# Kernel tuning notes

Measured on AMD Instinct MI355X. Metric: run time of the kernel, lower is better.

The kernel has to match this reference:

```python
import jax, jax.numpy as jnp
import numpy as np
import math

B, H, S, D = 2, 16, 2048, 128

def setup_inputs() -> dict:
    key = jax.random.key(0)
    kq, kk, kv, km = jax.random.split(key, 4)
    q = jax.random.normal(kq, (B, H, S, D), dtype=jnp.float32)
    k = jax.random.normal(kk, (B, H, S, D), dtype=jnp.float32)
    v = jax.random.normal(kv, (B, H, S, D), dtype=jnp.float32)
    mask = jax.random.randint(km, (1, 1, S, S), 0, 2, dtype=jnp.int32)
    return {"q": q, "k": k, "v": v, "mask": mask}

def reference(q, k, v, mask):
    head_dim = q.shape[-1]
    # scores: [B,H,Sq,Sk]
    scores = jnp.einsum('bhqd,bhkd->bhqk', q, k) / math.sqrt(head_dim)
    scores = jnp.where(mask == 0, jnp.float32(-1e10), scores)
    attn = jax.nn.softmax(scores, axis=-1)
    out = jnp.einsum('bhqk,bhkd->bhqd', attn, v)
    return out, attn
```

## Files before the change

kernel.cpp:

```cpp
#include <hip/hip_runtime.h>
#include <hip/hip_bf16.h>
#include <stdint.h>

#define SDIM 2048
#define DDIM 128
#define NKT  64

typedef __bf16 bf16x8 __attribute__((ext_vector_type(8)));
typedef float  f32x16 __attribute__((ext_vector_type(16)));

__global__ void build_bits_kernel(const int* __restrict__ mask, uint32_t* __restrict__ bitsT) {
  const int id   = blockIdx.x * 4 + (threadIdx.x >> 6);
  const int lane = threadIdx.x & 63;
  const int row  = id >> 5;
  const int kc   = id & 31;
  const int m = mask[(size_t)row * SDIM + kc * 64 + lane];
  const unsigned long long b = __ballot(m != 0);
  if (lane == 0)  bitsT[(size_t)(kc * 2    ) * SDIM + row] = (uint32_t)(b & 0xffffffffull);
  if (lane == 32) bitsT[(size_t)(kc * 2 + 1) * SDIM + row] = (uint32_t)(b >> 32);
}

__launch_bounds__(256, 2)
__global__ void attn_kernel(const float* __restrict__ qg, const float* __restrict__ kg,
                            const float* __restrict__ vg, const uint32_t* __restrict__ bitsT,
                            float* __restrict__ outg, float* __restrict__ attng) {
  __shared__ __align__(16) __bf16 KR[32 * 128];
  __shared__ __align__(16) __bf16 VTR[128 * 32];
  __shared__ __align__(16) __bf16 PR[4][32 * 32];
  __shared__ uint32_t MW[128];

  const int bid  = blockIdx.x;
  const int swzb = (bid & 7) * 64 + (bid >> 3);
  const int head = swzb >> 4;
  const int qb   = swzb & 15;
  const int tid  = threadIdx.x;
  const int wv   = tid >> 6;
  const int lane = tid & 63;
  const int col  = lane & 31;
  const int hi   = lane >> 5;

  const float* qh = qg + (size_t)head * SDIM * DDIM;
  const float* kh = kg + (size_t)head * SDIM * DDIM;
  const float* vh = vg + (size_t)head * SDIM * DDIM;
  float* outh  = outg  + (size_t)head * SDIM * DDIM;
  float* attnh = attng + (size_t)head * SDIM * SDIM;

  const int qrow0 = qb * 128 + wv * 32;
  const float cscale = 1.4426950408889634f * 0.08838834764831845f;
  const uint32_t lanebit = 1u << col;

  const int str = tid & 31;
  const int sdb = (tid >> 5) * 16;

  int rowl[16];
#pragma unroll
  for (int r = 0; r < 16; ++r) rowl[r] = wv * 32 + (r & 3) + 8 * (r >> 2) + 4 * hi;

  auto stage_k = [&](int kt) {
    const float* src = kh + (size_t)(kt * 32 + str) * DDIM + sdb;
    float4 a0 = *(const float4*)(src + 0);
    float4 a1 = *(const float4*)(src + 4);
    float4 a2 = *(const float4*)(src + 8);
    float4 a3 = *(const float4*)(src + 12);
    bf16x8 w0, w1;
    w0[0]=(__bf16)a0.x; w0[1]=(__bf16)a0.y; w0[2]=(__bf16)a0.z; w0[3]=(__bf16)a0.w;
    w0[4]=(__bf16)a1.x; w0[5]=(__bf16)a1.y; w0[6]=(__bf16)a1.z; w0[7]=(__bf16)a1.w;
    w1[0]=(__bf16)a2.x; w1[1]=(__bf16)a2.y; w1[2]=(__bf16)a2.z; w1[3]=(__bf16)a2.w;
    w1[4]=(__bf16)a3.x; w1[5]=(__bf16)a3.y; w1[6]=(__bf16)a3.z; w1[7]=(__bf16)a3.w;
    const int c0 = sdb >> 3;
    *(bf16x8*)&KR[str * 128 + (((c0    ) ^ (str & 15))) * 8] = w0;
    *(bf16x8*)&KR[str * 128 + (((c0 + 1) ^ (str & 15))) * 8] = w1;
  };
  auto stage_vt = [&](int kt) {
    const float* src = vh + (size_t)(kt * 32 + str) * DDIM + sdb;
    float4 a0 = *(const float4*)(src + 0);
    float4 a1 = *(const float4*)(src + 4);
    float4 a2 = *(const float4*)(src + 8);
    float4 a3 = *(const float4*)(src + 12);
    float vv[16] = {a0.x,a0.y,a0.z,a0.w, a1.x,a1.y,a1.z,a1.w,
                    a2.x,a2.y,a2.z,a2.w, a3.x,a3.y,a3.z,a3.w};
#pragma unroll
    for (int j = 0; j < 16; ++j) {
      const int d = sdb + j;
      VTR[d * 32 + (((str >> 3) ^ ((d >> 1) & 3)) << 3) + (str & 7)] = (__bf16)vv[j];
    }
  };
  auto stage_mw = [&](int kt) {
    if (tid < 128) MW[tid] = bitsT[(size_t)kt * SDIM + qb * 128 + tid];
  };

  bf16x8 qf[8];
#pragma unroll
  for (int s = 0; s < 8; ++s) {
    const float* src = qh + (size_t)(qrow0 + col) * DDIM + s * 16 + hi * 8;
    float4 f0 = *(const float4*)(src);
    float4 f1 = *(const float4*)(src + 4);
    bf16x8 t;
    t[0]=(__bf16)f0.x; t[1]=(__bf16)f0.y; t[2]=(__bf16)f0.z; t[3]=(__bf16)f0.w;
    t[4]=(__bf16)f1.x; t[5]=(__bf16)f1.y; t[6]=(__bf16)f1.z; t[7]=(__bf16)f1.w;
    qf[s] = t;
  }

  float lsum[16];
#pragma unroll
  for (int r = 0; r < 16; ++r) lsum[r] = 0.0f;

  for (int kt = 0; kt < NKT; ++kt) {
    stage_k(kt);
    stage_mw(kt);
    __syncthreads();

    f32x16 sacc = {};
#pragma unroll
    for (int s = 0; s < 8; ++s) {
      bf16x8 kf = *(const bf16x8*)&KR[col * 128 + (((s * 2 + hi) ^ (col & 15))) * 8];
      sacc = __builtin_amdgcn_mfma_f32_32x32x16_bf16(qf[s], kf, sacc, 0, 0, 0);
    }
#pragma unroll
    for (int r = 0; r < 16; ++r) {
      const uint32_t w = MW[rowl[r]];
      float pe = __builtin_amdgcn_exp2f(sacc[r] * cscale);
      pe = (w & lanebit) ? pe : 0.0f;
      lsum[r] += pe;
    }
    __syncthreads();
  }

  float loglr[16];
#pragma unroll
  for (int r = 0; r < 16; ++r) {
    float t = lsum[r];
    t += __shfl_xor(t, 1);
    t += __shfl_xor(t, 2);
    t += __shfl_xor(t, 4);
    t += __shfl_xor(t, 8);
    t += __shfl_xor(t, 16);
    loglr[r] = __builtin_amdgcn_logf(fmaxf(t, 1e-30f));
  }

  f32x16 oacc[4] = {};

  for (int kt = 0; kt < NKT; ++kt) {
    stage_k(kt);
    stage_vt(kt);
    stage_mw(kt);
    __syncthreads();

    f32x16 sacc = {};
#pragma unroll
    for (int s = 0; s < 8; ++s) {
      bf16x8 kf = *(const bf16x8*)&KR[col * 128 + (((s * 2 + hi) ^ (col & 15))) * 8];
      sacc = __builtin_amdgcn_mfma_f32_32x32x16_bf16(qf[s], kf, sacc, 0, 0, 0);
    }

#pragma unroll
    for (int r = 0; r < 16; ++r) {
      const uint32_t w = MW[rowl[r]];
      float pn = __builtin_amdgcn_exp2f(fmaf(sacc[r], cscale, -loglr[r]));
      pn = (w & lanebit) ? pn : 0.0f;
      __builtin_nontemporal_store(pn,
          &attnh[(size_t)(qb * 128 + rowl[r]) * SDIM + kt * 32 + col]);
      const int qr = rowl[r] - wv * 32;
      PR[wv][qr * 32 + (((col >> 3) ^ ((qr >> 1) & 3)) << 3) + (col & 7)] = (__bf16)pn;
    }

#pragma unroll
    for (int ks = 0; ks < 2; ++ks) {
      bf16x8 pf = *(const bf16x8*)&PR[wv][col * 32 + (((ks * 2 + hi) ^ ((col >> 1) & 3)) << 3)];
#pragma unroll
      for (int dt = 0; dt < 4; ++dt) {
        const int d = dt * 32 + col;
        bf16x8 vf = *(const bf16x8*)&VTR[d * 32 + (((ks * 2 + hi) ^ ((d >> 1) & 3)) << 3)];
        oacc[dt] = __builtin_amdgcn_mfma_f32_32x32x16_bf16(pf, vf, oacc[dt], 0, 0, 0);
      }
    }
    __syncthreads();
  }

#pragma unroll
  for (int dt = 0; dt < 4; ++dt) {
#pragma unroll
    for (int r = 0; r < 16; ++r) {
      __builtin_nontemporal_store(oacc[dt][r],
          &outh[(size_t)(qb * 128 + rowl[r]) * DDIM + dt * 32 + col]);
    }
  }
}

extern "C" void kernel_launch(void* const* d_in, const int* in_sizes, int n_in,
                              void* d_out, int out_size, void* d_ws, size_t ws_size,
                              hipStream_t stream) {
  const float* q   = (const float*)d_in[0];
  const float* k   = (const float*)d_in[1];
  const float* v   = (const float*)d_in[2];
  const int*  mask = (const int*)d_in[3];
  float* outp  = (float*)d_out;
  float* attnp = outp + (size_t)2 * 16 * 2048 * 128;
  uint32_t* bitsT = (uint32_t*)d_ws;

  hipLaunchKernelGGL(build_bits_kernel, dim3(2048 * 32 / 4), dim3(256), 0, stream, mask, bitsT);
  hipLaunchKernelGGL(attn_kernel, dim3(512), dim3(256), 0, stream,
                     q, k, v, bitsT, outp, attnp);
}
```

Before: 911.0 us.

## Double-buffer K/V/mask tiles with register prefetch and 64-key tiles

Doubles the key tile from 32 to 64 rows and adds double-buffered LDS for K, transposed V and the mask words. The next tile's global loads are issued into registers before the current tile's MFMA work and written to the alternate buffer afterwards, so each iteration needs one barrier instead of two. This is meant to hide global-load latency behind compute and halve barrier count. In exchange LDS use roughly quadruples for K/V and register pressure grows from the prefetch registers, which may reduce occupancy under launch_bounds(256,2).

Result: slower. 1.035 ms (+13.6%).

```diff
diff --git a/kernel.cpp b/kernel.cpp
--- a/kernel.cpp
+++ b/kernel.cpp
@@ -4,7 +4,7 @@
 
 #define SDIM 2048
 #define DDIM 128
-#define NKT  64
+#define NT   32
 
 typedef __bf16 bf16x8 __attribute__((ext_vector_type(8)));
 typedef float  f32x16 __attribute__((ext_vector_type(16)));
@@ -20,14 +20,21 @@
   if (lane == 32) bitsT[(size_t)(kc * 2 + 1) * SDIM + row] = (uint32_t)(b >> 32);
 }
 
+__device__ inline bf16x8 pack8(const float4& a, const float4& b) {
+  bf16x8 t;
+  t[0]=(__bf16)a.x; t[1]=(__bf16)a.y; t[2]=(__bf16)a.z; t[3]=(__bf16)a.w;
+  t[4]=(__bf16)b.x; t[5]=(__bf16)b.y; t[6]=(__bf16)b.z; t[7]=(__bf16)b.w;
+  return t;
+}
+
 __launch_bounds__(256, 2)
 __global__ void attn_kernel(const float* __restrict__ qg, const float* __restrict__ kg,
                             const float* __restrict__ vg, const uint32_t* __restrict__ bitsT,
                             float* __restrict__ outg, float* __restrict__ attng) {
-  __shared__ __align__(16) __bf16 KR[32 * 128];
-  __shared__ __align__(16) __bf16 VTR[128 * 32];
+  __shared__ __align__(16) __bf16 KR[2][64 * 128];
+  __shared__ __align__(16) __bf16 VTR[2][128 * 64];
   __shared__ __align__(16) __bf16 PR[4][32 * 32];
-  __shared__ uint32_t MW[128];
+  __shared__ uint32_t MW[2][2][128];
 
   const int bid  = blockIdx.x;
   const int swzb = (bid & 7) * 64 + (bid >> 3);
@@ -56,38 +63,56 @@
 #pragma unroll
   for (int r = 0; r < 16; ++r) rowl[r] = wv * 32 + (r & 3) + 8 * (r >> 2) + 4 * hi;
 
-  auto stage_k = [&](int kt) {
-    const float* src = kh + (size_t)(kt * 32 + str) * DDIM + sdb;
-    float4 a0 = *(const float4*)(src + 0);
-    float4 a1 = *(const float4*)(src + 4);
-    float4 a2 = *(const float4*)(src + 8);
-    float4 a3 = *(const float4*)(src + 12);
-    bf16x8 w0, w1;
-    w0[0]=(__bf16)a0.x; w0[1]=(__bf16)a0.y; w0[2]=(__bf16)a0.z; w0[3]=(__bf16)a0.w;
-    w0[4]=(__bf16)a1.x; w0[5]=(__bf16)a1.y; w0[6]=(__bf16)a1.z; w0[7]=(__bf16)a1.w;
-    w1[0]=(__bf16)a2.x; w1[1]=(__bf16)a2.y; w1[2]=(__bf16)a2.z; w1[3]=(__bf16)a2.w;
-    w1[4]=(__bf16)a3.x; w1[5]=(__bf16)a3.y; w1[6]=(__bf16)a3.z; w1[7]=(__bf16)a3.w;
-    const int c0 = sdb >> 3;
-    *(bf16x8*)&KR[str * 128 + (((c0    ) ^ (str & 15))) * 8] = w0;
-    *(bf16x8*)&KR[str * 128 + (((c0 + 1) ^ (str & 15))) * 8] = w1;
-  };
-  auto stage_vt = [&](int kt) {
-    const float* src = vh + (size_t)(kt * 32 + str) * DDIM + sdb;
-    float4 a0 = *(const float4*)(src + 0);
-    float4 a1 = *(const float4*)(src + 4);
-    float4 a2 = *(const float4*)(src + 8);
-    float4 a3 = *(const float4*)(src + 12);
-    float vv[16] = {a0.x,a0.y,a0.z,a0.w, a1.x,a1.y,a1.z,a1.w,
-                    a2.x,a2.y,a2.z,a2.w, a3.x,a3.y,a3.z,a3.w};
-#pragma unroll
-    for (int j = 0; j < 16; ++j) {
-      const int d = sdb + j;
-      VTR[d * 32 + (((str >> 3) ^ ((d >> 1) & 3)) << 3) + (str & 7)] = (__bf16)vv[j];
-    }
-  };
-  auto stage_mw = [&](int kt) {
-    if (tid < 128) MW[tid] = bitsT[(size_t)kt * SDIM + qb * 128 + tid];
-  };
+  float4 kr[2][4], vrg[2][4];
+  uint32_t mwreg;
+
+  auto issueK = [&](int kt) {
+#pragma unroll
+    for (int rh = 0; rh < 2; ++rh) {
+      const float* s = kh + (size_t)(kt * 64 + rh * 32 + str) * DDIM + sdb;
+      kr[rh][0] = *(const float4*)(s + 0);
+      kr[rh][1] = *(const float4*)(s + 4);
+      kr[rh][2] = *(const float4*)(s + 8);
+      kr[rh][3] = *(const float4*)(s + 12);
+    }
+  };
+  auto issueV = [&](int kt) {
+#pragma unroll
+    for (int rh = 0; rh < 2; ++rh) {
+      const float* s = vh + (size_t)(kt * 64 + rh * 32 + str) * DDIM + sdb;
+      vrg[rh][0] = *(const float4*)(s + 0);
+      vrg[rh][1] = *(const float4*)(s + 4);
+      vrg[rh][2] = *(const float4*)(s + 8);
+      vrg[rh][3] = *(const float4*)(s + 12);
+    }
+  };
+  auto issueM = [&](int kt) {
+    mwreg = bitsT[(size_t)(kt * 2 + (tid >> 7)) * SDIM + qb * 128 + (tid & 127)];
+  };
+  auto writeK = [&](int b) {
+#pragma unroll
+    for (int rh = 0; rh < 2; ++rh) {
+      const int row = rh * 32 + str;
+      const int c0 = sdb >> 3;
+      *(bf16x8*)&KR[b][row * 128 + (((c0    ) ^ (str & 15))) * 8] = pack8(kr[rh][0], kr[rh][1]);
+      *(bf16x8*)&KR[b][row * 128 + (((c0 + 1) ^ (str & 15))) * 8] = pack8(kr[rh][2], kr[rh][3]);
+    }
+  };
+  auto writeV = [&](int b) {
+#pragma unroll
+    for (int rh = 0; rh < 2; ++rh) {
+      float vv[16] = {vrg[rh][0].x, vrg[rh][0].y, vrg[rh][0].z, vrg[rh][0].w,
+                      vrg[rh][1].x, vrg[rh][1].y, vrg[rh][1].z, vrg[rh][1].w,
+                      vrg[rh][2].x, vrg[rh][2].y, vrg[rh][2].z, vrg[rh][2].w,
+                      vrg[rh][3].x, vrg[rh][3].y, vrg[rh][3].z, vrg[rh][3].w};
+#pragma unroll
+      for (int j = 0; j < 16; ++j) {
+        const int d = sdb + j;
+        VTR[b][d * 64 + rh * 32 + (((str >> 3) ^ ((d >> 1) & 3)) << 3) + (str & 7)] = (__bf16)vv[j];
+      }
+    }
+  };
+  auto writeM = [&](int b) { MW[b][tid >> 7][tid & 127] = mwreg; };
 
   bf16x8 qf[8];
 #pragma unroll
@@ -95,35 +120,39 @@
     const float* src = qh + (size_t)(qrow0 + col) * DDIM + s * 16 + hi * 8;
     float4 f0 = *(const float4*)(src);
     float4 f1 = *(const float4*)(src + 4);
-    bf16x8 t;
-    t[0]=(__bf16)f0.x; t[1]=(__bf16)f0.y; t[2]=(__bf16)f0.z; t[3]=(__bf16)f0.w;
-    t[4]=(__bf16)f1.x; t[5]=(__bf16)f1.y; t[6]=(__bf16)f1.z; t[7]=(__bf16)f1.w;
-    qf[s] = t;
+    qf[s] = pack8(f0, f1);
   }
 
   float lsum[16];
 #pragma unroll
   for (int r = 0; r < 16; ++r) lsum[r] = 0.0f;
 
-  for (int kt = 0; kt < NKT; ++kt) {
-    stage_k(kt);
-    stage_mw(kt);
+  issueK(0); issueM(0);
+  writeK(0); writeM(0);
+  __syncthreads();
+  int cur = 0;
+  for (int kt = 0; kt < NT; ++kt) {
+    const bool pf = (kt + 1 < NT);
+    if (pf) { issueK(kt + 1); issueM(kt + 1); }
+#pragma unroll
+    for (int h = 0; h < 2; ++h) {
+      f32x16 sacc = {};
+#pragma unroll
+      for (int s = 0; s < 8; ++s) {
+        bf16x8 kf = *(const bf16x8*)&KR[cur][(h * 32 + col) * 128 + (((s * 2 + hi) ^ (col & 15))) * 8];
+        sacc = __builtin_amdgcn_mfma_f32_32x32x16_bf16(qf[s], kf, sacc, 0, 0, 0);
+      }
+#pragma unroll
+      for (int r = 0; r < 16; ++r) {
+        const uint32_t w = MW[cur][h][rowl[r]];
+        float pe = __builtin_amdgcn_exp2f(sacc[r] * cscale);
+        pe = (w & lanebit) ? pe : 0.0f;
+        lsum[r] += pe;
+      }
+    }
+    if (pf) { writeK(cur ^ 1); writeM(cur ^ 1); }
     __syncthreads();
-
-    f32x16 sacc = {};
-#pragma unroll
-    for (int s = 0; s < 8; ++s) {
-      bf16x8 kf = *(const bf16x8*)&KR[col * 128 + (((s * 2 + hi) ^ (col & 15))) * 8];
-      sacc = __builtin_amdgcn_mfma_f32_32x32x16_bf16(qf[s], kf, sacc, 0, 0, 0);
-    }
-#pragma unroll
-    for (int r = 0; r < 16; ++r) {
-      const uint32_t w = MW[rowl[r]];
-      float pe = __builtin_amdgcn_exp2f(sacc[r] * cscale);
-      pe = (w & lanebit) ? pe : 0.0f;
-      lsum[r] += pe;
-    }
-    __syncthreads();
+    cur ^= 1;
   }
 
   float loglr[16];
@@ -140,41 +169,45 @@
 
   f32x16 oacc[4] = {};
 
-  for (int kt = 0; kt < NKT; ++kt) {
-    stage_k(kt);
-    stage_vt(kt);
-    stage_mw(kt);
+  issueK(0); issueV(0); issueM(0);
+  writeK(0); writeV(0); writeM(0);
+  __syncthreads();
+  cur = 0;
+  for (int kt = 0; kt < NT; ++kt) {
+    const bool pf = (kt + 1 < NT);
+    if (pf) { issueK(kt + 1); issueV(kt + 1); issueM(kt + 1); }
+#pragma unroll
+    for (int h = 0; h < 2; ++h) {
+      f32x16 sacc = {};
+#pragma unroll
+      for (int s = 0; s < 8; ++s) {
+        bf16x8 kf = *(const bf16x8*)&KR[cur][(h * 32 + col) * 128 + (((s * 2 + hi) ^ (col & 15))) * 8];
+        sacc = __builtin_amdgcn_mfma_f32_32x32x16_bf16(qf[s], kf, sacc, 0, 0, 0);
+      }
+#pragma unroll
+      for (int r = 0; r < 16; ++r) {
+        const uint32_t w = MW[cur][h][rowl[r]];
+        float pn = __builtin_amdgcn_exp2f(fmaf(sacc[r], cscale, -loglr[r]));
+        pn = (w & lanebit) ? pn : 0.0f;
+        __builtin_nontemporal_store(pn,
+            &attnh[(size_t)(qb * 128 + rowl[r]) * SDIM + kt * 64 + h * 32 + col]);
+        const int qr = rowl[r] - wv * 32;
+        PR[wv][qr * 32 + (((col >> 3) ^ ((qr >> 1) & 3)) << 3) + (col & 7)] = (__bf16)pn;
+      }
+#pragma unroll
+      for (int ks = 0; ks < 2; ++ks) {
+        bf16x8 pfr = *(const bf16x8*)&PR[wv][col * 32 + (((ks * 2 + hi) ^ ((col >> 1) & 3)) << 3)];
+#pragma unroll
+        for (int dt = 0; dt < 4; ++dt) {
+          const int d = dt * 32 + col;
+          bf16x8 vf = *(const bf16x8*)&VTR[cur][d * 64 + h * 32 + (((ks * 2 + hi) ^ ((d >> 1) & 3)) << 3)];
+          oacc[dt] = __builtin_amdgcn_mfma_f32_32x32x16_bf16(pfr, vf, oacc[dt], 0, 0, 0);
+        }
+      }
+    }
+    if (pf) { writeK(cur ^ 1); writeV(cur ^ 1); writeM(cur ^ 1); }
     __syncthreads();
-
-    f32x16 sacc = {};
-#pragma unroll
-    for (int s = 0; s < 8; ++s) {
-      bf16x8 kf = *(const bf16x8*)&KR[col * 128 + (((s * 2 + hi) ^ (col & 15))) * 8];
-      sacc = __builtin_amdgcn_mfma_f32_32x32x16_bf16(qf[s], kf, sacc, 0, 0, 0);
-    }
-
-#pragma unroll
-    for (int r = 0; r < 16; ++r) {
-      const uint32_t w = MW[rowl[r]];
-      float pn = __builtin_amdgcn_exp2f(fmaf(sacc[r], cscale, -loglr[r]));
-      pn = (w & lanebit) ? pn : 0.0f;
-      __builtin_nontemporal_store(pn,
-          &attnh[(size_t)(qb * 128 + rowl[r]) * SDIM + kt * 32 + col]);
-      const int qr = rowl[r] - wv * 32;
-      PR[wv][qr * 32 + (((col >> 3) ^ ((qr >> 1) & 3)) << 3) + (col & 7)] = (__bf16)pn;
-    }
-
-#pragma unroll
-    for (int ks = 0; ks < 2; ++ks) {
-      bf16x8 pf = *(const bf16x8*)&PR[wv][col * 32 + (((ks * 2 + hi) ^ ((col >> 1) & 3)) << 3)];
-#pragma unroll
-      for (int dt = 0; dt < 4; ++dt) {
-        const int d = dt * 32 + col;
-        bf16x8 vf = *(const bf16x8*)&VTR[d * 32 + (((ks * 2 + hi) ^ ((d >> 1) & 3)) << 3)];
-        oacc[dt] = __builtin_amdgcn_mfma_f32_32x32x16_bf16(pf, vf, oacc[dt], 0, 0, 0);
-      }
-    }
-    __syncthreads();
+    cur ^= 1;
   }
 
 #pragma unroll
```
